# Kernel optimization log

Measured on AMD Instinct MI355X. Metric: run time of the kernel, lower is better.

Reference implementation:

```python
import jax, jax.numpy as jnp
from jax import lax
import numpy as np

B, M = 16384, 200            # flattened batch (B*TT), tokens per observation
NUM_LAYERS, GW, GH = 22, 11, 11
CNN_CH, HIDDEN = 128, 512
ACTION_NVEC = (9, 10)

MAX_VEC = jnp.array([9.0, 1.0, 1.0, 10.0, 3.0, 254.0, 1.0, 1.0, 235.0, 8.0, 9.0,
                     250.0, 29.0, 1.0, 1.0, 8.0, 1.0, 1.0, 6.0, 3.0, 1.0, 2.0],
                    jnp.float32)[None, :, None, None]  # [1,22,1,1]


def setup_inputs() -> dict:
    key = jax.random.key(0)
    ks = jax.random.split(key, 16)
    # compose coords byte so x,y nibbles are valid grid indices (0..10)
    xs = jax.random.randint(ks[0], (B, M), 0, GW)
    ys = jax.random.randint(ks[1], (B, M), 0, GH)
    coords = xs * 16 + ys
    atr = jax.random.randint(ks[2], (B, M), 0, NUM_LAYERS)
    val = jax.random.randint(ks[3], (B, M), 0, 11)
    observations = jnp.stack([coords, atr, val], axis=-1).astype(jnp.int32)  # [B,M,3]

    def nrm(k, shape, std=0.02):
        return (jax.random.normal(k, shape, jnp.float32) * std)

    return {
        "observations": observations,
        "conv1_w": nrm(ks[4], (CNN_CH, NUM_LAYERS, 5, 5)),
        "conv1_b": jnp.zeros((CNN_CH,), jnp.float32),
        "conv2_w": nrm(ks[5], (CNN_CH, CNN_CH, 3, 3)),
        "conv2_b": jnp.zeros((CNN_CH,), jnp.float32),
        "fc_w": nrm(ks[6], (HIDDEN // 2, CNN_CH)),
        "fc_b": jnp.zeros((HIDDEN // 2,), jnp.float32),
        "self_w": nrm(ks[7], (HIDDEN // 2, NUM_LAYERS)),
        "self_b": jnp.zeros((HIDDEN // 2,), jnp.float32),
        "actor0_w": nrm(ks[8], (ACTION_NVEC[0], HIDDEN), std=0.01),
        "actor0_b": jnp.zeros((ACTION_NVEC[0],), jnp.float32),
        "actor1_w": nrm(ks[9], (ACTION_NVEC[1], HIDDEN), std=0.01),
        "actor1_b": jnp.zeros((ACTION_NVEC[1],), jnp.float32),
        "value_w": nrm(ks[10], (1, HIDDEN)),
        "value_b": jnp.zeros((1,), jnp.float32),
    }


def reference(observations, conv1_w, conv1_b, conv2_w, conv2_b, fc_w, fc_b,
              self_w, self_b, actor0_w, actor0_b, actor1_w, actor1_b,
              value_w, value_b):
    obs = jnp.where(observations == 255, 0, observations)
    coords = obs[..., 0]
    xs = (coords >> 4) & 15
    ys = coords & 15
    atr = obs[..., 1]
    vals = obs[..., 2].astype(jnp.float32)           # [B,M]
    Bt = obs.shape[0]
    b_idx = jnp.broadcast_to(jnp.arange(Bt)[:, None], vals.shape)
    # masked scatter into dense grid (all tokens valid after 255->0 clamp)
    box = jnp.zeros((Bt, NUM_LAYERS, GW, GH), jnp.float32)
    box = box.at[b_idx, atr, xs, ys].set(vals, mode="drop")
    feats = box / MAX_VEC                            # [B,22,11,11]

    self_f = jax.nn.relu(feats[:, :, 5, 5] @ self_w.T + self_b)  # [B,256]

    dn = ("NCHW", "OIHW", "NCHW")
    h = lax.conv_general_dilated(feats, conv1_w, (3, 3), "VALID", dimension_numbers=dn)
    h = jax.nn.relu(h + conv1_b[None, :, None, None])            # [B,128,3,3]
    h = lax.conv_general_dilated(h, conv2_w, (1, 1), "VALID", dimension_numbers=dn)
    h = jax.nn.relu(h + conv2_b[None, :, None, None])            # [B,128,1,1]
    h = h.reshape(Bt, -1)
    cnn_f = jax.nn.relu(h @ fc_w.T + fc_b)                       # [B,256]

    hidden = jnp.concatenate([self_f, cnn_f], axis=1)            # [B,512]
    logits0 = hidden @ actor0_w.T + actor0_b
    logits1 = hidden @ actor1_w.T + actor1_b
    value = hidden @ value_w.T + value_b
    return (logits0, logits1, value)
```

## Files before the change

### kernel.cpp

```cpp
#include <hip/hip_runtime.h>

typedef unsigned short u16;
typedef __attribute__((ext_vector_type(8))) short short8;
typedef __attribute__((ext_vector_type(4))) float f32x4;

#define MFMA16(a, b, c) __builtin_amdgcn_mfma_f32_16x16x32_bf16((a), (b), (c), 0, 0, 0)

__device__ __forceinline__ u16 f2bf(float f) {
    unsigned u = __float_as_uint(f);
    unsigned r = (u + 0x7FFFu + ((u >> 16) & 1u)) >> 16;
    return (u16)r;
}

__device__ const float MAXV[22] = {9.f, 1.f, 1.f, 10.f, 3.f, 254.f, 1.f, 1.f, 235.f, 8.f, 9.f,
                                   250.f, 29.f, 1.f, 1.f, 8.f, 1.f, 1.f, 6.f, 3.f, 1.f, 2.f};

__global__ void prep_kernel(
    const float* c1w, const float* c1b, const float* c2w, const float* c2b,
    const float* fcw, const float* fcb, const float* sfw, const float* sfb,
    const float* a0w, const float* a0b, const float* a1w, const float* a1b,
    const float* vw, const float* vb,
    u16* W1F, u16* W2F, u16* FCF, u16* SELFF, u16* HEADF, float* BIAS)
{
    int idx = blockIdx.x * 256 + threadIdx.x;
    if (idx < 73728) {
        int grp = idx >> 9, off = idx & 511;
        int g = grp / 18, ks = grp - g * 18;
        int l = off >> 3, e = off & 7;
        int n = g * 16 + (l & 15);
        int k = ks * 32 + ((l >> 4) << 3) + e;
        float v = 0.f;
        if (k < 550) { int c = k / 25; v = c1w[n * 550 + k] * (1.0f / MAXV[c]); }
        W1F[idx] = f2bf(v);
    } else if (idx < 221184) {
        int j = idx - 73728;
        int grp = j >> 9, off = j & 511;
        int g = grp / 36, ks = grp - g * 36;
        int l = off >> 3, e = off & 7;
        int oc = g * 16 + (l & 15);
        int k = ks * 32 + ((l >> 4) << 3) + e;
        W2F[j] = f2bf(c2w[oc * 1152 + (k & 127) * 9 + (k >> 7)]);
    } else if (idx < 253952) {
        int j = idx - 221184;
        int grp = j >> 9, off = j & 511;
        int g = grp >> 2, kc = grp & 3;
        int l = off >> 3, e = off & 7;
        int n = g * 16 + (l & 15);
        int k = kc * 32 + ((l >> 4) << 3) + e;
        FCF[j] = f2bf(fcw[n * 128 + k]);
    } else if (idx < 262144) {
        int j = idx - 253952;
        int g = j >> 9, off = j & 511;
        int l = off >> 3, e = off & 7;
        int n = g * 16 + (l & 15);
        int k = ((l >> 4) << 3) + e;
        float v = (k < 22) ? sfw[n * 22 + k] * (1.0f / MAXV[k]) : 0.f;
        SELFF[j] = f2bf(v);
    } else if (idx < 278528) {
        int j = idx - 262144;
        int grp = j >> 9, off = j & 511;
        int g = grp >> 4, ks = grp & 15;
        int l = off >> 3, e = off & 7;
        int n = g * 16 + (l & 15);
        int k = ks * 32 + ((l >> 4) << 3) + e;
        float v = 0.f;
        if (n < 9) v = a0w[n * 512 + k];
        else if (n < 19) v = a1w[(n - 9) * 512 + k];
        else if (n == 19) v = vw[k];
        HEADF[j] = f2bf(v);
    } else if (idx < 279328) {
        int j = idx - 278528;
        float v = 0.f;
        if (j < 128) v = c1b[j];
        else if (j < 256) v = c2b[j - 128];
        else if (j < 512) v = fcb[j - 256];
        else if (j < 768) v = sfb[j - 512];
        else {
            int j2 = j - 768;
            if (j2 < 9) v = a0b[j2]; else if (j2 < 19) v = a1b[j2 - 9]; else if (j2 == 19) v = vb[0];
        }
        BIAS[j] = v;
    }
}

__global__ __launch_bounds__(256, 3) void k12_kernel(
    const int* __restrict__ obs, const u16* __restrict__ W1F,
    const float* __restrict__ BIAS, u16* __restrict__ h1F, u16* __restrict__ s22g)
{
    __shared__ __align__(16) u16 A[36 * 576];
    __shared__ __align__(16) int box[2664];
    __shared__ u16 s22[128];
    const int tid = threadIdx.x, w = tid >> 6, l = tid & 63;
    const int s0 = blockIdx.x * 4;

    int tok[4][3];
    if (tid < 200) {
        #pragma unroll
        for (int p = 0; p < 4; ++p) {
            const int* tp = obs + (long)(s0 + p) * 600 + tid * 3;
            tok[p][0] = tp[0]; tok[p][1] = tp[1]; tok[p][2] = tp[2];
        }
    }

    {
        short8 z = {0, 0, 0, 0, 0, 0, 0, 0};
        for (int i = tid; i < 2592; i += 256) *(short8*)(A + i * 8) = z;
        int4 zz = {0, 0, 0, 0};
        for (int i = tid; i < 666; i += 256) ((int4*)box)[i] = zz;
        if (tid < 128) s22[tid] = 0;
    }
    __syncthreads();

    #pragma unroll
    for (int p = 0; p < 4; ++p) {
        int ce = 0, en = 0, va = 0, xa = 0, ya = 0, aa = 0, ok = 0;
        if (tid < 200) {
            int c = tok[p][0], a = tok[p][1], v = tok[p][2];
            c = (c == 255) ? 0 : c; a = (a == 255) ? 0 : a; v = (v == 255) ? 0 : v;
            int xs = (c >> 4) & 15, ys = c & 15;
            ok = ((unsigned)a < 22u) & (xs < 11) & (ys < 11);
            ce = a * 121 + xs * 11 + ys;
            en = ((p + 1) << 16) | (tid << 8) | (v & 255);
            va = v; xa = xs; ya = ys; aa = a;
            if (ok) atomicMax(&box[ce], en);
        }
        __syncthreads();
        if (ok && box[ce] == en) {
            u16 bv = f2bf((float)va);
            if (xa == 5 && ya == 5) s22[p * 32 + aa] = bv;
            int bcol = aa * 25;
            #pragma unroll
            for (int ox = 0; ox < 3; ++ox) {
                int kx = xa - 3 * ox;
                if ((unsigned)kx > 4u) continue;
                #pragma unroll
                for (int oy = 0; oy < 3; ++oy) {
                    int ky = ya - 3 * oy;
                    if ((unsigned)ky > 4u) continue;
                    int row = p * 9 + ox * 3 + oy;
                    int byte = ((row * 576 + bcol + kx * 5 + ky) << 1) ^ ((row & 7) << 4);
                    *(u16*)((char*)A + byte) = bv;
                }
            }
        }
        __syncthreads();
    }
    if (tid < 128) s22g[s0 * 32 + tid] = s22[tid];

    int Aoff[3][2];
    #pragma unroll
    for (int mt = 0; mt < 3; ++mt) {
        int row = mt * 16 + (l & 15);
        row = row < 36 ? row : 35;
        int koff = (l >> 4) << 3;
        Aoff[mt][0] = ((row * 576 + koff) << 1) ^ ((row & 7) << 4);
        Aoff[mt][1] = ((row * 576 + 32 + koff) << 1) ^ ((row & 7) << 4);
    }
    const u16* Wp0 = W1F + ((w * 2 + 0) * 18 << 9) + l * 8;
    const u16* Wp1 = W1F + ((w * 2 + 1) * 18 << 9) + l * 8;

    f32x4 acc[3][2];
    const f32x4 fz = {0.f, 0.f, 0.f, 0.f};
    #pragma unroll
    for (int i = 0; i < 3; ++i) { acc[i][0] = fz; acc[i][1] = fz; }

    short8 cb0 = *(const short8*)(Wp0);
    short8 cb1 = *(const short8*)(Wp1);
    short8 nb0 = *(const short8*)(Wp0 + 512);
    short8 nb1 = *(const short8*)(Wp1 + 512);
    __builtin_amdgcn_s_setprio(1);
    #pragma unroll
    for (int ks = 0; ks < 18; ++ks) {
        short8 t0 = cb0, t1 = cb1;
        if (ks < 16) {
            t0 = *(const short8*)(Wp0 + (ks + 2) * 512);
            t1 = *(const short8*)(Wp1 + (ks + 2) * 512);
        }
        short8 a0 = *(const short8*)((const char*)A + Aoff[0][ks & 1] + (ks >> 1) * 128);
        short8 a1 = *(const short8*)((const char*)A + Aoff[1][ks & 1] + (ks >> 1) * 128);
        short8 a2 = *(const short8*)((const char*)A + Aoff[2][ks & 1] + (ks >> 1) * 128);
        acc[0][0] = MFMA16(a0, cb0, acc[0][0]);
        acc[0][1] = MFMA16(a0, cb1, acc[0][1]);
        acc[1][0] = MFMA16(a1, cb0, acc[1][0]);
        acc[1][1] = MFMA16(a1, cb1, acc[1][1]);
        acc[2][0] = MFMA16(a2, cb0, acc[2][0]);
        acc[2][1] = MFMA16(a2, cb1, acc[2][1]);
        cb0 = nb0; cb1 = nb1; nb0 = t0; nb1 = t1;
    }
    __builtin_amdgcn_s_setprio(0);

    u16* R = (u16*)box;
    #pragma unroll
    for (int mt = 0; mt < 3; ++mt) {
        #pragma unroll
        for (int nt = 0; nt < 2; ++nt) {
            int col = w * 32 + nt * 16 + (l & 15);
            float bias = BIAS[col];
            int hif = nt * 2 + ((l & 15) >> 3);
            int ef = l & 7;
            #pragma unroll
            for (int r = 0; r < 4; ++r) {
                int row = mt * 16 + ((l >> 4) << 2) + r;
                if (row < 36) {
                    int ds = row / 9;
                    int pos = row - ds * 9;
                    int ks = pos * 4 + w;
                    float v = acc[mt][nt][r] + bias;
                    v = v > 0.f ? v : 0.f;
                    R[(ks * 16 + hif * 4 + ds) * 8 + ef] = f2bf(v);
                }
            }
        }
    }
    __syncthreads();
    {
        const long Cbase = (long)(s0 >> 4) * 18432 + (s0 & 15) * 8;
        #pragma unroll
        for (int q = 0; q < 3; ++q) {
            int slot = tid + q * 256;
            if (slot < 576) {
                int ks = slot >> 4, lf = slot & 15;
                *(short8*)(h1F + Cbase + ks * 512 + (lf >> 2) * 128 + (lf & 3) * 8) =
                    *(const short8*)(R + slot * 8);
            }
        }
    }
}

__global__ __launch_bounds__(256, 2) void k3_kernel(
    const u16* __restrict__ h1F, const u16* __restrict__ s22g,
    const u16* __restrict__ W2F, const u16* __restrict__ FCF,
    const u16* __restrict__ SELFF, const u16* __restrict__ HEADF,
    const float* __restrict__ BIAS, float* __restrict__ out, int B)
{
    __shared__ __align__(16) u16 A3[32 * 136];
    __shared__ __align__(16) u16 HID[32 * 520];
    const int tid = threadIdx.x, w = tid >> 6, l = tid & 63;
    const int s0 = blockIdx.x * 32;
    const int sb = blockIdx.x * 2;
    const float* c2b = BIAS + 128;
    const float* fcb = BIAS + 256;
    const float* sfb = BIAS + 512;
    const float* hdb = BIAS + 768;
    const f32x4 fz = {0.f, 0.f, 0.f, 0.f};

    f32x4 acc[2][2];
    acc[0][0] = fz; acc[0][1] = fz; acc[1][0] = fz; acc[1][1] = fz;
    const u16* A0p = h1F + (long)(sb + 0) * 18432 + l * 8;
    const u16* A1p = h1F + (long)(sb + 1) * 18432 + l * 8;
    const u16* B0p = W2F + ((w * 2 + 0) * 36 << 9) + l * 8;
    const u16* B1p = W2F + ((w * 2 + 1) * 36 << 9) + l * 8;

    short8 ca0 = *(const short8*)(A0p), ca1 = *(const short8*)(A1p);
    short8 cb0 = *(const short8*)(B0p), cb1 = *(const short8*)(B1p);
    short8 na0 = *(const short8*)(A0p + 512), na1 = *(const short8*)(A1p + 512);
    short8 nb0 = *(const short8*)(B0p + 512), nb1 = *(const short8*)(B1p + 512);
    __builtin_amdgcn_s_setprio(1);
    #pragma unroll
    for (int ks = 0; ks < 36; ++ks) {
        short8 t0 = ca0, t1 = ca1, t2 = cb0, t3 = cb1;
        if (ks < 34) {
            t0 = *(const short8*)(A0p + (ks + 2) * 512);
            t1 = *(const short8*)(A1p + (ks + 2) * 512);
            t2 = *(const short8*)(B0p + (ks + 2) * 512);
            t3 = *(const short8*)(B1p + (ks + 2) * 512);
        }
        acc[0][0] = MFMA16(ca0, cb0, acc[0][0]);
        acc[0][1] = MFMA16(ca0, cb1, acc[0][1]);
        acc[1][0] = MFMA16(ca1, cb0, acc[1][0]);
        acc[1][1] = MFMA16(ca1, cb1, acc[1][1]);
        ca0 = na0; ca1 = na1; cb0 = nb0; cb1 = nb1;
        na0 = t0; na1 = t1; nb0 = t2; nb1 = t3;
    }
    __builtin_amdgcn_s_setprio(0);
    {
        #pragma unroll
        for (int mt = 0; mt < 2; ++mt)
            #pragma unroll
            for (int nt = 0; nt < 2; ++nt) {
                int col = w * 32 + nt * 16 + (l & 15);
                float bias = c2b[col];
                #pragma unroll
                for (int r = 0; r < 4; ++r) {
                    int row = mt * 16 + ((l >> 4) << 2) + r;
                    float v = acc[mt][nt][r] + bias; v = v > 0.f ? v : 0.f;
                    A3[row * 136 + col] = f2bf(v);
                }
            }
    }
    __syncthreads();

    f32x4 acc8[2][4];
    #pragma unroll
    for (int i = 0; i < 2; ++i)
        #pragma unroll
        for (int j = 0; j < 4; ++j) acc8[i][j] = fz;
    #pragma unroll
    for (int kc = 0; kc < 4; ++kc) {
        short8 bf[4];
        #pragma unroll
        for (int nt = 0; nt < 4; ++nt)
            bf[nt] = *(const short8*)(FCF + (((w * 4 + nt) * 4 + kc) << 9) + l * 8);
        #pragma unroll
        for (int mt = 0; mt < 2; ++mt) {
            short8 a = *(const short8*)(A3 + (mt * 16 + (l & 15)) * 136 + kc * 32 + ((l >> 4) << 3));
            #pragma unroll
            for (int nt = 0; nt < 4; ++nt) acc8[mt][nt] = MFMA16(a, bf[nt], acc8[mt][nt]);
        }
    }
    {
        #pragma unroll
        for (int mt = 0; mt < 2; ++mt)
            #pragma unroll
            for (int nt = 0; nt < 4; ++nt) {
                int col = w * 64 + nt * 16 + (l & 15);
                float bias = fcb[col];
                #pragma unroll
                for (int r = 0; r < 4; ++r) {
                    int row = mt * 16 + ((l >> 4) << 2) + r;
                    float v = acc8[mt][nt][r] + bias; v = v > 0.f ? v : 0.f;
                    HID[row * 520 + 256 + col] = f2bf(v);
                }
            }
    }

    {
        f32x4 acc9[2][4];
        #pragma unroll
        for (int i = 0; i < 2; ++i)
            #pragma unroll
            for (int j = 0; j < 4; ++j) acc9[i][j] = fz;
        short8 bs[4];
        #pragma unroll
        for (int nt = 0; nt < 4; ++nt)
            bs[nt] = *(const short8*)(SELFF + ((w * 4 + nt) << 9) + l * 8);
        #pragma unroll
        for (int mt = 0; mt < 2; ++mt) {
            short8 a = *(const short8*)(s22g + (s0 + mt * 16 + (l & 15)) * 32 + ((l >> 4) << 3));
            #pragma unroll
            for (int nt = 0; nt < 4; ++nt) acc9[mt][nt] = MFMA16(a, bs[nt], acc9[mt][nt]);
        }
        #pragma unroll
        for (int mt = 0; mt < 2; ++mt)
            #pragma unroll
            for (int nt = 0; nt < 4; ++nt) {
                int col = w * 64 + nt * 16 + (l & 15);
                float bias = sfb[col];
                #pragma unroll
                for (int r = 0; r < 4; ++r) {
                    int row = mt * 16 + ((l >> 4) << 2) + r;
                    float v = acc9[mt][nt][r] + bias; v = v > 0.f ? v : 0.f;
                    HID[row * 520 + col] = f2bf(v);
                }
            }
    }
    __syncthreads();

    f32x4 hacc = fz;
    const int rt = w & 1, ct = w >> 1;
    #pragma unroll
    for (int ks = 0; ks < 16; ++ks) {
        short8 a = *(const short8*)(HID + (rt * 16 + (l & 15)) * 520 + ks * 32 + ((l >> 4) << 3));
        short8 b = *(const short8*)(HEADF + ((ct * 16 + ks) << 9) + l * 8);
        hacc = MFMA16(a, b, hacc);
    }
    #pragma unroll
    for (int r = 0; r < 4; ++r) {
        int srow = s0 + rt * 16 + ((l >> 4) << 2) + r;
        int col = ct * 16 + (l & 15);
        float v = hacc[r] + hdb[col];
        if (col < 9) out[(long)srow * 9 + col] = v;
        else if (col < 19) out[(long)B * 9 + (long)srow * 10 + (col - 9)] = v;
        else if (col == 19) out[(long)B * 19 + srow] = v;
    }
}

extern "C" void kernel_launch(void* const* d_in, const int* in_sizes, int n_in,
                              void* d_out, int out_size, void* d_ws, size_t ws_size,
                              hipStream_t stream)
{
    const int*   obs = (const int*)d_in[0];
    const float* c1w = (const float*)d_in[1];
    const float* c1b = (const float*)d_in[2];
    const float* c2w = (const float*)d_in[3];
    const float* c2b = (const float*)d_in[4];
    const float* fcw = (const float*)d_in[5];
    const float* fcb = (const float*)d_in[6];
    const float* sfw = (const float*)d_in[7];
    const float* sfb = (const float*)d_in[8];
    const float* a0w = (const float*)d_in[9];
    const float* a0b = (const float*)d_in[10];
    const float* a1w = (const float*)d_in[11];
    const float* a1b = (const float*)d_in[12];
    const float* vw  = (const float*)d_in[13];
    const float* vb  = (const float*)d_in[14];
    const int B = in_sizes[0] / 600;

    char* ws = (char*)d_ws;
    u16*   W1F   = (u16*)(ws + 0);
    u16*   W2F   = (u16*)(ws + 147456);
    u16*   FCF   = (u16*)(ws + 442368);
    u16*   SELFF = (u16*)(ws + 507904);
    u16*   HEADF = (u16*)(ws + 524288);
    float* BIAS  = (float*)(ws + 557056);
    u16*   s22g  = (u16*)(ws + 560256);
    u16*   h1F   = (u16*)(ws + 560256 + (size_t)B * 64);

    prep_kernel<<<1092, 256, 0, stream>>>(c1w, c1b, c2w, c2b, fcw, fcb, sfw, sfb,
                                          a0w, a0b, a1w, a1b, vw, vb,
                                          W1F, W2F, FCF, SELFF, HEADF, BIAS);
    k12_kernel<<<B / 4, 256, 0, stream>>>(obs, W1F, BIAS, h1F, s22g);
    k3_kernel<<<B / 32, 256, 0, stream>>>(h1F, s22g, W2F, FCF, SELFF, HEADF, BIAS,
                                          (float*)d_out, B);
}
```

Before: 75.94 us.

## Give each wave its own scatter sample and halve k3 tile to 16 rows

In k12, each wave now owns one sample: it scatters its tokens into a per-wave scratch region that serves first as the dedup box and then as the im2col tile. This replaces the four block-wide barrier rounds with wave-local work and shrinks shared memory. In k3, each block processes 16 samples instead of 32, uses a 3-deep prefetch pipeline, and raises the occupancy target to 4 blocks; only two waves run the head GEMM. The trade-off is less weight reuse per block in k3 and reliance on wave-internal ordering of LDS atomics without a barrier.

```diff
diff --git a/kernel.cpp b/kernel.cpp
--- a/kernel.cpp
+++ b/kernel.cpp
@@ -87,74 +87,78 @@
     const int* __restrict__ obs, const u16* __restrict__ W1F,
     const float* __restrict__ BIAS, u16* __restrict__ h1F, u16* __restrict__ s22g)
 {
-    __shared__ __align__(16) u16 A[36 * 576];
-    __shared__ __align__(16) int box[2664];
+    __shared__ __align__(16) u16 Ablk[4 * 5328];
     __shared__ u16 s22[128];
     const int tid = threadIdx.x, w = tid >> 6, l = tid & 63;
     const int s0 = blockIdx.x * 4;
-
-    int tok[4][3];
-    if (tid < 200) {
-        #pragma unroll
-        for (int p = 0; p < 4; ++p) {
-            const int* tp = obs + (long)(s0 + p) * 600 + tid * 3;
-            tok[p][0] = tp[0]; tok[p][1] = tp[1]; tok[p][2] = tp[2];
-        }
-    }
-
-    {
-        short8 z = {0, 0, 0, 0, 0, 0, 0, 0};
-        for (int i = tid; i < 2592; i += 256) *(short8*)(A + i * 8) = z;
-        int4 zz = {0, 0, 0, 0};
-        for (int i = tid; i < 666; i += 256) ((int4*)box)[i] = zz;
-        if (tid < 128) s22[tid] = 0;
-    }
-    __syncthreads();
-
-    #pragma unroll
-    for (int p = 0; p < 4; ++p) {
-        int ce = 0, en = 0, va = 0, xa = 0, ya = 0, aa = 0, ok = 0;
-        if (tid < 200) {
-            int c = tok[p][0], a = tok[p][1], v = tok[p][2];
-            c = (c == 255) ? 0 : c; a = (a == 255) ? 0 : a; v = (v == 255) ? 0 : v;
-            int xs = (c >> 4) & 15, ys = c & 15;
-            ok = ((unsigned)a < 22u) & (xs < 11) & (ys < 11);
-            ce = a * 121 + xs * 11 + ys;
-            en = ((p + 1) << 16) | (tid << 8) | (v & 255);
-            va = v; xa = xs; ya = ys; aa = a;
-            if (ok) atomicMax(&box[ce], en);
-        }
-        __syncthreads();
-        if (ok && box[ce] == en) {
-            u16 bv = f2bf((float)va);
-            if (xa == 5 && ya == 5) s22[p * 32 + aa] = bv;
-            int bcol = aa * 25;
+    const short8 z8 = {0, 0, 0, 0, 0, 0, 0, 0};
+
+    const int* myobs = obs + (long)(s0 + w) * 600;
+    int tk[4][3];
+    #pragma unroll
+    for (int r = 0; r < 4; ++r) {
+        int m = r * 64 + l; m = m < 200 ? m : 0;
+        tk[r][0] = myobs[m * 3]; tk[r][1] = myobs[m * 3 + 1]; tk[r][2] = myobs[m * 3 + 2];
+    }
+    if (l < 32) s22[w * 32 + l] = 0;
+
+    u16* blk = Ablk + w * 5328;
+    for (int i = l; i < 666; i += 64) *(short8*)(blk + i * 8) = z8;
+
+    int* boxW = (int*)blk;
+    int ce[4], en[4], ok[4], va[4], xa[4], ya[4], aa[4], win[4];
+    #pragma unroll
+    for (int r = 0; r < 4; ++r) {
+        int m = r * 64 + l;
+        int c = tk[r][0], a = tk[r][1], v = tk[r][2];
+        c = (c == 255) ? 0 : c; a = (a == 255) ? 0 : a; v = (v == 255) ? 0 : v;
+        int xs = (c >> 4) & 15, ys = c & 15;
+        ok[r] = (m < 200) & ((unsigned)a < 22u) & (xs < 11) & (ys < 11);
+        ce[r] = ok[r] ? (a * 121 + xs * 11 + ys) : 0;
+        en[r] = ((m + 1) << 8) | (v & 255);
+        va[r] = v; xa[r] = xs; ya[r] = ys; aa[r] = a;
+        if (ok[r]) atomicMax(&boxW[ce[r]], en[r]);
+    }
+    __builtin_amdgcn_sched_barrier(0);
+    #pragma unroll
+    for (int r = 0; r < 4; ++r) win[r] = ok[r] & (boxW[ce[r]] == en[r]);
+    __builtin_amdgcn_sched_barrier(0);
+    for (int i = l; i < 666; i += 64) *(short8*)(blk + i * 8) = z8;
+    __builtin_amdgcn_sched_barrier(0);
+    #pragma unroll
+    for (int r = 0; r < 4; ++r) {
+        if (win[r]) {
+            u16 bv = f2bf((float)va[r]);
+            if (xa[r] == 5 && ya[r] == 5) s22[w * 32 + aa[r]] = bv;
+            int bcol = aa[r] * 25;
             #pragma unroll
             for (int ox = 0; ox < 3; ++ox) {
-                int kx = xa - 3 * ox;
+                int kx = xa[r] - 3 * ox;
                 if ((unsigned)kx > 4u) continue;
                 #pragma unroll
                 for (int oy = 0; oy < 3; ++oy) {
-                    int ky = ya - 3 * oy;
+                    int ky = ya[r] - 3 * oy;
                     if ((unsigned)ky > 4u) continue;
-                    int row = p * 9 + ox * 3 + oy;
-                    int byte = ((row * 576 + bcol + kx * 5 + ky) << 1) ^ ((row & 7) << 4);
-                    *(u16*)((char*)A + byte) = bv;
+                    int pos = ox * 3 + oy;
+                    int row = w * 9 + pos;
+                    int off = (((pos * 576 + bcol + kx * 5 + ky)) << 1) ^ ((row & 7) << 4);
+                    *(u16*)((char*)blk + off) = bv;
                 }
             }
         }
-        __syncthreads();
-    }
-    if (tid < 128) s22g[s0 * 32 + tid] = s22[tid];
-
-    int Aoff[3][2];
+    }
+    if (l < 32) s22g[(s0 + w) * 32 + l] = s22[w * 32 + l];
+    __syncthreads();
+
+    int addr[3][2];
     #pragma unroll
     for (int mt = 0; mt < 3; ++mt) {
         int row = mt * 16 + (l & 15);
         row = row < 36 ? row : 35;
+        int ls = row / 9, pos = row - ls * 9;
         int koff = (l >> 4) << 3;
-        Aoff[mt][0] = ((row * 576 + koff) << 1) ^ ((row & 7) << 4);
-        Aoff[mt][1] = ((row * 576 + 32 + koff) << 1) ^ ((row & 7) << 4);
+        addr[mt][0] = ls * 10656 + (((pos * 576 + koff) << 1) ^ ((row & 7) << 4));
+        addr[mt][1] = ls * 10656 + (((pos * 576 + 32 + koff) << 1) ^ ((row & 7) << 4));
     }
     const u16* Wp0 = W1F + ((w * 2 + 0) * 18 << 9) + l * 8;
     const u16* Wp1 = W1F + ((w * 2 + 1) * 18 << 9) + l * 8;
@@ -176,9 +180,9 @@
             t0 = *(const short8*)(Wp0 + (ks + 2) * 512);
             t1 = *(const short8*)(Wp1 + (ks + 2) * 512);
         }
-        short8 a0 = *(const short8*)((const char*)A + Aoff[0][ks & 1] + (ks >> 1) * 128);
-        short8 a1 = *(const short8*)((const char*)A + Aoff[1][ks & 1] + (ks >> 1) * 128);
-        short8 a2 = *(const short8*)((const char*)A + Aoff[2][ks & 1] + (ks >> 1) * 128);
+        short8 a0 = *(const short8*)((const char*)Ablk + addr[0][ks & 1] + (ks >> 1) * 128);
+        short8 a1 = *(const short8*)((const char*)Ablk + addr[1][ks & 1] + (ks >> 1) * 128);
+        short8 a2 = *(const short8*)((const char*)Ablk + addr[2][ks & 1] + (ks >> 1) * 128);
         acc[0][0] = MFMA16(a0, cb0, acc[0][0]);
         acc[0][1] = MFMA16(a0, cb1, acc[0][1]);
         acc[1][0] = MFMA16(a1, cb0, acc[1][0]);
@@ -188,8 +192,9 @@
         cb0 = nb0; cb1 = nb1; nb0 = t0; nb1 = t1;
     }
     __builtin_amdgcn_s_setprio(0);
-
-    u16* R = (u16*)box;
+    __syncthreads();
+
+    u16* R = Ablk;
     #pragma unroll
     for (int mt = 0; mt < 3; ++mt) {
         #pragma unroll
@@ -227,151 +232,133 @@
     }
 }
 
-__global__ __launch_bounds__(256, 2) void k3_kernel(
+__global__ __launch_bounds__(256, 4) void k3_kernel(
     const u16* __restrict__ h1F, const u16* __restrict__ s22g,
     const u16* __restrict__ W2F, const u16* __restrict__ FCF,
     const u16* __restrict__ SELFF, const u16* __restrict__ HEADF,
     const float* __restrict__ BIAS, float* __restrict__ out, int B)
 {
-    __shared__ __align__(16) u16 A3[32 * 136];
-    __shared__ __align__(16) u16 HID[32 * 520];
+    __shared__ __align__(16) u16 A3[16 * 136];
+    __shared__ __align__(16) u16 HID[16 * 520];
     const int tid = threadIdx.x, w = tid >> 6, l = tid & 63;
-    const int s0 = blockIdx.x * 32;
-    const int sb = blockIdx.x * 2;
+    const int s0 = blockIdx.x * 16;
     const float* c2b = BIAS + 128;
     const float* fcb = BIAS + 256;
     const float* sfb = BIAS + 512;
     const float* hdb = BIAS + 768;
     const f32x4 fz = {0.f, 0.f, 0.f, 0.f};
 
-    f32x4 acc[2][2];
-    acc[0][0] = fz; acc[0][1] = fz; acc[1][0] = fz; acc[1][1] = fz;
-    const u16* A0p = h1F + (long)(sb + 0) * 18432 + l * 8;
-    const u16* A1p = h1F + (long)(sb + 1) * 18432 + l * 8;
+    const u16* Ap  = h1F + (long)blockIdx.x * 18432 + l * 8;
     const u16* B0p = W2F + ((w * 2 + 0) * 36 << 9) + l * 8;
     const u16* B1p = W2F + ((w * 2 + 1) * 36 << 9) + l * 8;
-
-    short8 ca0 = *(const short8*)(A0p), ca1 = *(const short8*)(A1p);
-    short8 cb0 = *(const short8*)(B0p), cb1 = *(const short8*)(B1p);
-    short8 na0 = *(const short8*)(A0p + 512), na1 = *(const short8*)(A1p + 512);
-    short8 nb0 = *(const short8*)(B0p + 512), nb1 = *(const short8*)(B1p + 512);
+    f32x4 acc0 = fz, acc1 = fz;
+    short8 pa[3], pb0[3], pb1[3];
+    #pragma unroll
+    for (int d = 0; d < 3; ++d) {
+        pa[d]  = *(const short8*)(Ap + d * 512);
+        pb0[d] = *(const short8*)(B0p + d * 512);
+        pb1[d] = *(const short8*)(B1p + d * 512);
+    }
     __builtin_amdgcn_s_setprio(1);
     #pragma unroll
-    for (int ks = 0; ks < 36; ++ks) {
-        short8 t0 = ca0, t1 = ca1, t2 = cb0, t3 = cb1;
-        if (ks < 34) {
-            t0 = *(const short8*)(A0p + (ks + 2) * 512);
-            t1 = *(const short8*)(A1p + (ks + 2) * 512);
-            t2 = *(const short8*)(B0p + (ks + 2) * 512);
-            t3 = *(const short8*)(B1p + (ks + 2) * 512);
-        }
-        acc[0][0] = MFMA16(ca0, cb0, acc[0][0]);
-        acc[0][1] = MFMA16(ca0, cb1, acc[0][1]);
-        acc[1][0] = MFMA16(ca1, cb0, acc[1][0]);
-        acc[1][1] = MFMA16(ca1, cb1, acc[1][1]);
-        ca0 = na0; ca1 = na1; cb0 = nb0; cb1 = nb1;
-        na0 = t0; na1 = t1; nb0 = t2; nb1 = t3;
+    for (int g = 0; g < 12; ++g) {
+        #pragma unroll
+        for (int d = 0; d < 3; ++d) {
+            int ks = g * 3 + d;
+            short8 a = pa[d], b0 = pb0[d], b1 = pb1[d];
+            if (ks < 33) {
+                pa[d]  = *(const short8*)(Ap + (ks + 3) * 512);
+                pb0[d] = *(const short8*)(B0p + (ks + 3) * 512);
+                pb1[d] = *(const short8*)(B1p + (ks + 3) * 512);
+            }
+            acc0 = MFMA16(a, b0, acc0);
+            acc1 = MFMA16(a, b1, acc1);
+        }
     }
     __builtin_amdgcn_s_setprio(0);
     {
         #pragma unroll
-        for (int mt = 0; mt < 2; ++mt)
+        for (int nt = 0; nt < 2; ++nt) {
+            int col = w * 32 + nt * 16 + (l & 15);
+            float bias = c2b[col];
+            const f32x4& a4 = nt ? acc1 : acc0;
             #pragma unroll
-            for (int nt = 0; nt < 2; ++nt) {
-                int col = w * 32 + nt * 16 + (l & 15);
-                float bias = c2b[col];
-                #pragma unroll
-                for (int r = 0; r < 4; ++r) {
-                    int row = mt * 16 + ((l >> 4) << 2) + r;
-                    float v = acc[mt][nt][r] + bias; v = v > 0.f ? v : 0.f;
-                    A3[row * 136 + col] = f2bf(v);
-                }
-            }
+            for (int r = 0; r < 4; ++r) {
+                int row = ((l >> 4) << 2) + r;
+                float v = a4[r] + bias; v = v > 0.f ? v : 0.f;
+                A3[row * 136 + col] = f2bf(v);
+            }
+        }
     }
     __syncthreads();
 
-    f32x4 acc8[2][4];
-    #pragma unroll
-    for (int i = 0; i < 2; ++i)
-        #pragma unroll
-        for (int j = 0; j < 4; ++j) acc8[i][j] = fz;
+    f32x4 acc8[4];
+    #pragma unroll
+    for (int j = 0; j < 4; ++j) acc8[j] = fz;
     #pragma unroll
     for (int kc = 0; kc < 4; ++kc) {
         short8 bf[4];
         #pragma unroll
         for (int nt = 0; nt < 4; ++nt)
             bf[nt] = *(const short8*)(FCF + (((w * 4 + nt) * 4 + kc) << 9) + l * 8);
-        #pragma unroll
-        for (int mt = 0; mt < 2; ++mt) {
-            short8 a = *(const short8*)(A3 + (mt * 16 + (l & 15)) * 136 + kc * 32 + ((l >> 4) << 3));
-            #pragma unroll
-            for (int nt = 0; nt < 4; ++nt) acc8[mt][nt] = MFMA16(a, bf[nt], acc8[mt][nt]);
-        }
-    }
+        short8 a = *(const short8*)(A3 + (l & 15) * 136 + kc * 32 + ((l >> 4) << 3));
+        #pragma unroll
+        for (int nt = 0; nt < 4; ++nt) acc8[nt] = MFMA16(a, bf[nt], acc8[nt]);
+    }
+    #pragma unroll
+    for (int nt = 0; nt < 4; ++nt) {
+        int col = w * 64 + nt * 16 + (l & 15);
+        float bias = fcb[col];
+        #pragma unroll
+        for (int r = 0; r < 4; ++r) {
+            int row = ((l >> 4) << 2) + r;
+            float v = acc8[nt][r] + bias; v = v > 0.f ? v : 0.f;
+            HID[row * 520 + 256 + col] = f2bf(v);
+        }
+    }
+
     {
-        #pragma unroll
-        for (int mt = 0; mt < 2; ++mt)
-            #pragma unroll
-            for (int nt = 0; nt < 4; ++nt) {
-                int col = w * 64 + nt * 16 + (l & 15);
-                float bias = fcb[col];
-                #pragma unroll
-                for (int r = 0; r < 4; ++r) {
-                    int row = mt * 16 + ((l >> 4) << 2) + r;
-                    float v = acc8[mt][nt][r] + bias; v = v > 0.f ? v : 0.f;
-                    HID[row * 520 + 256 + col] = f2bf(v);
-                }
-            }
-    }
-
-    {
-        f32x4 acc9[2][4];
-        #pragma unroll
-        for (int i = 0; i < 2; ++i)
-            #pragma unroll
-            for (int j = 0; j < 4; ++j) acc9[i][j] = fz;
+        f32x4 acc9[4];
+        #pragma unroll
+        for (int j = 0; j < 4; ++j) acc9[j] = fz;
         short8 bs[4];
         #pragma unroll
         for (int nt = 0; nt < 4; ++nt)
             bs[nt] = *(const short8*)(SELFF + ((w * 4 + nt) << 9) + l * 8);
-        #pragma unroll
-        for (int mt = 0; mt < 2; ++mt) {
-            short8 a = *(const short8*)(s22g + (s0 + mt * 16 + (l & 15)) * 32 + ((l >> 4) << 3));
+        short8 a = *(const short8*)(s22g + (s0 + (l & 15)) * 32 + ((l >> 4) << 3));
+        #pragma unroll
+        for (int nt = 0; nt < 4; ++nt) acc9[nt] = MFMA16(a, bs[nt], acc9[nt]);
+        #pragma unroll
+        for (int nt = 0; nt < 4; ++nt) {
+            int col = w * 64 + nt * 16 + (l & 15);
+            float bias = sfb[col];
             #pragma unroll
-            for (int nt = 0; nt < 4; ++nt) acc9[mt][nt] = MFMA16(a, bs[nt], acc9[mt][nt]);
-        }
-        #pragma unroll
-        for (int mt = 0; mt < 2; ++mt)
-            #pragma unroll
-            for (int nt = 0; nt < 4; ++nt) {
-                int col = w * 64 + nt * 16 + (l & 15);
-                float bias = sfb[col];
-                #pragma unroll
-                for (int r = 0; r < 4; ++r) {
-                    int row = mt * 16 + ((l >> 4) << 2) + r;
-                    float v = acc9[mt][nt][r] + bias; v = v > 0.f ? v : 0.f;
-                    HID[row * 520 + col] = f2bf(v);
-                }
-            }
+            for (int r = 0; r < 4; ++r) {
+                int row = ((l >> 4) << 2) + r;
+                float v = acc9[nt][r] + bias; v = v > 0.f ? v : 0.f;
+                HID[row * 520 + col] = f2bf(v);
+            }
+        }
     }
     __syncthreads();
 
-    f32x4 hacc = fz;
-    const int rt = w & 1, ct = w >> 1;
-    #pragma unroll
-    for (int ks = 0; ks < 16; ++ks) {
-        short8 a = *(const short8*)(HID + (rt * 16 + (l & 15)) * 520 + ks * 32 + ((l >> 4) << 3));
-        short8 b = *(const short8*)(HEADF + ((ct * 16 + ks) << 9) + l * 8);
-        hacc = MFMA16(a, b, hacc);
-    }
-    #pragma unroll
-    for (int r = 0; r < 4; ++r) {
-        int srow = s0 + rt * 16 + ((l >> 4) << 2) + r;
-        int col = ct * 16 + (l & 15);
-        float v = hacc[r] + hdb[col];
-        if (col < 9) out[(long)srow * 9 + col] = v;
-        else if (col < 19) out[(long)B * 9 + (long)srow * 10 + (col - 9)] = v;
-        else if (col == 19) out[(long)B * 19 + srow] = v;
+    if (w < 2) {
+        f32x4 hacc = fz;
+        #pragma unroll
+        for (int ks = 0; ks < 16; ++ks) {
+            short8 a = *(const short8*)(HID + (l & 15) * 520 + ks * 32 + ((l >> 4) << 3));
+            short8 b = *(const short8*)(HEADF + ((w * 16 + ks) << 9) + l * 8);
+            hacc = MFMA16(a, b, hacc);
+        }
+        #pragma unroll
+        for (int r = 0; r < 4; ++r) {
+            int srow = s0 + ((l >> 4) << 2) + r;
+            int col = w * 16 + (l & 15);
+            float v = hacc[r] + hdb[col];
+            if (col < 9) out[(long)srow * 9 + col] = v;
+            else if (col < 19) out[(long)B * 9 + (long)srow * 10 + (col - 9)] = v;
+            else if (col == 19) out[(long)B * 19 + srow] = v;
+        }
     }
 }
 
@@ -410,6 +397,6 @@
                                           a0w, a0b, a1w, a1b, vw, vb,
                                           W1F, W2F, FCF, SELFF, HEADF, BIAS);
     k12_kernel<<<B / 4, 256, 0, stream>>>(obs, W1F, BIAS, h1F, s22g);
-    k3_kernel<<<B / 32, 256, 0, stream>>>(h1F, s22g, W2F, FCF, SELFF, HEADF, BIAS,
+    k3_kernel<<<B / 16, 256, 0, stream>>>(h1F, s22g, W2F, FCF, SELFF, HEADF, BIAS,
                                           (float*)d_out, B);
 }
```

Result: slower. 79.31 us (+4.4%).

## Split conv2 and FC/head stages into separate kernels via global MFMA-layout buffer

Applied to the files above, without the earlier changes.

Splits the fused conv2+FC+self+head kernel into two kernels. The first does the conv2 GEMM and writes the ReLU'd bf16 activations to a global buffer in MFMA fragment layout. The second processes 16 samples per block with higher occupancy for the FC, self and head GEMMs. The aim is more parallelism and occupancy in the tail stages, at the cost of an extra launch and a global round trip of the intermediate activations.

```diff
diff --git a/kernel.cpp b/kernel.cpp
--- a/kernel.cpp
+++ b/kernel.cpp
@@ -227,25 +227,17 @@
     }
 }
 
-__global__ __launch_bounds__(256, 2) void k3_kernel(
-    const u16* __restrict__ h1F, const u16* __restrict__ s22g,
-    const u16* __restrict__ W2F, const u16* __restrict__ FCF,
-    const u16* __restrict__ SELFF, const u16* __restrict__ HEADF,
-    const float* __restrict__ BIAS, float* __restrict__ out, int B)
+__global__ __launch_bounds__(256, 2) void k3a_kernel(
+    const u16* __restrict__ h1F, const u16* __restrict__ W2F,
+    const float* __restrict__ BIAS, u16* __restrict__ a3F)
 {
-    __shared__ __align__(16) u16 A3[32 * 136];
-    __shared__ __align__(16) u16 HID[32 * 520];
     const int tid = threadIdx.x, w = tid >> 6, l = tid & 63;
-    const int s0 = blockIdx.x * 32;
-    const int sb = blockIdx.x * 2;
+    const int sb = blockIdx.x * 2, s0 = blockIdx.x * 32;
     const float* c2b = BIAS + 128;
-    const float* fcb = BIAS + 256;
-    const float* sfb = BIAS + 512;
-    const float* hdb = BIAS + 768;
     const f32x4 fz = {0.f, 0.f, 0.f, 0.f};
-
     f32x4 acc[2][2];
     acc[0][0] = fz; acc[0][1] = fz; acc[1][0] = fz; acc[1][1] = fz;
+
     const u16* A0p = h1F + (long)(sb + 0) * 18432 + l * 8;
     const u16* A1p = h1F + (long)(sb + 1) * 18432 + l * 8;
     const u16* B0p = W2F + ((w * 2 + 0) * 36 << 9) + l * 8;
@@ -273,105 +265,105 @@
         na0 = t0; na1 = t1; nb0 = t2; nb1 = t3;
     }
     __builtin_amdgcn_s_setprio(0);
+
+    #pragma unroll
+    for (int mt = 0; mt < 2; ++mt) {
+        #pragma unroll
+        for (int nt = 0; nt < 2; ++nt) {
+            int col = w * 32 + nt * 16 + (l & 15);
+            float bias = c2b[col];
+            #pragma unroll
+            for (int r = 0; r < 4; ++r) {
+                int row = mt * 16 + ((l >> 4) << 2) + r;
+                int s = s0 + row;
+                float v = acc[mt][nt][r] + bias; v = v > 0.f ? v : 0.f;
+                long ad = (long)(s >> 4) * 2048 + (col >> 5) * 512 +
+                          (s & 15) * 8 + (((col >> 3) & 3) << 7) + (col & 7);
+                a3F[ad] = f2bf(v);
+            }
+        }
+    }
+}
+
+__global__ __launch_bounds__(256, 4) void k3b_kernel(
+    const u16* __restrict__ a3F, const u16* __restrict__ s22g,
+    const u16* __restrict__ FCF, const u16* __restrict__ SELFF,
+    const u16* __restrict__ HEADF, const float* __restrict__ BIAS,
+    float* __restrict__ out, int B)
+{
+    __shared__ __align__(16) u16 HID[16 * 520];
+    const int tid = threadIdx.x, w = tid >> 6, l = tid & 63;
+    const int s0 = blockIdx.x * 16;
+    const float* fcb = BIAS + 256;
+    const float* sfb = BIAS + 512;
+    const float* hdb = BIAS + 768;
+    const f32x4 fz = {0.f, 0.f, 0.f, 0.f};
+
+    f32x4 acc8[4];
+    #pragma unroll
+    for (int j = 0; j < 4; ++j) acc8[j] = fz;
+    #pragma unroll
+    for (int kc = 0; kc < 4; ++kc) {
+        short8 a = *(const short8*)(a3F + (long)blockIdx.x * 2048 + kc * 512 + l * 8);
+        #pragma unroll
+        for (int nt = 0; nt < 4; ++nt) {
+            short8 bf = *(const short8*)(FCF + (((w * 4 + nt) * 4 + kc) << 9) + l * 8);
+            acc8[nt] = MFMA16(a, bf, acc8[nt]);
+        }
+    }
+    #pragma unroll
+    for (int nt = 0; nt < 4; ++nt) {
+        int col = w * 64 + nt * 16 + (l & 15);
+        float bias = fcb[col];
+        #pragma unroll
+        for (int r = 0; r < 4; ++r) {
+            int row = ((l >> 4) << 2) + r;
+            float v = acc8[nt][r] + bias; v = v > 0.f ? v : 0.f;
+            HID[row * 520 + 256 + col] = f2bf(v);
+        }
+    }
+
     {
-        #pragma unroll
-        for (int mt = 0; mt < 2; ++mt)
+        f32x4 acc9[4];
+        #pragma unroll
+        for (int j = 0; j < 4; ++j) acc9[j] = fz;
+        short8 a = *(const short8*)(s22g + (s0 + (l & 15)) * 32 + ((l >> 4) << 3));
+        #pragma unroll
+        for (int nt = 0; nt < 4; ++nt) {
+            short8 bs = *(const short8*)(SELFF + ((w * 4 + nt) << 9) + l * 8);
+            acc9[nt] = MFMA16(a, bs, acc9[nt]);
+        }
+        #pragma unroll
+        for (int nt = 0; nt < 4; ++nt) {
+            int col = w * 64 + nt * 16 + (l & 15);
+            float bias = sfb[col];
             #pragma unroll
-            for (int nt = 0; nt < 2; ++nt) {
-                int col = w * 32 + nt * 16 + (l & 15);
-                float bias = c2b[col];
-                #pragma unroll
-                for (int r = 0; r < 4; ++r) {
-                    int row = mt * 16 + ((l >> 4) << 2) + r;
-                    float v = acc[mt][nt][r] + bias; v = v > 0.f ? v : 0.f;
-                    A3[row * 136 + col] = f2bf(v);
-                }
+            for (int r = 0; r < 4; ++r) {
+                int row = ((l >> 4) << 2) + r;
+                float v = acc9[nt][r] + bias; v = v > 0.f ? v : 0.f;
+                HID[row * 520 + col] = f2bf(v);
             }
+        }
     }
     __syncthreads();
 
-    f32x4 acc8[2][4];
-    #pragma unroll
-    for (int i = 0; i < 2; ++i)
-        #pragma unroll
-        for (int j = 0; j < 4; ++j) acc8[i][j] = fz;
-    #pragma unroll
-    for (int kc = 0; kc < 4; ++kc) {
-        short8 bf[4];
-        #pragma unroll
-        for (int nt = 0; nt < 4; ++nt)
-            bf[nt] = *(const short8*)(FCF + (((w * 4 + nt) * 4 + kc) << 9) + l * 8);
-        #pragma unroll
-        for (int mt = 0; mt < 2; ++mt) {
-            short8 a = *(const short8*)(A3 + (mt * 16 + (l & 15)) * 136 + kc * 32 + ((l >> 4) << 3));
-            #pragma unroll
-            for (int nt = 0; nt < 4; ++nt) acc8[mt][nt] = MFMA16(a, bf[nt], acc8[mt][nt]);
-        }
-    }
-    {
-        #pragma unroll
-        for (int mt = 0; mt < 2; ++mt)
-            #pragma unroll
-            for (int nt = 0; nt < 4; ++nt) {
-                int col = w * 64 + nt * 16 + (l & 15);
-                float bias = fcb[col];
-                #pragma unroll
-                for (int r = 0; r < 4; ++r) {
-                    int row = mt * 16 + ((l >> 4) << 2) + r;
-                    float v = acc8[mt][nt][r] + bias; v = v > 0.f ? v : 0.f;
-                    HID[row * 520 + 256 + col] = f2bf(v);
-                }
-            }
-    }
-
-    {
-        f32x4 acc9[2][4];
-        #pragma unroll
-        for (int i = 0; i < 2; ++i)
-            #pragma unroll
-            for (int j = 0; j < 4; ++j) acc9[i][j] = fz;
-        short8 bs[4];
-        #pragma unroll
-        for (int nt = 0; nt < 4; ++nt)
-            bs[nt] = *(const short8*)(SELFF + ((w * 4 + nt) << 9) + l * 8);
-        #pragma unroll
-        for (int mt = 0; mt < 2; ++mt) {
-            short8 a = *(const short8*)(s22g + (s0 + mt * 16 + (l & 15)) * 32 + ((l >> 4) << 3));
-            #pragma unroll
-            for (int nt = 0; nt < 4; ++nt) acc9[mt][nt] = MFMA16(a, bs[nt], acc9[mt][nt]);
-        }
-        #pragma unroll
-        for (int mt = 0; mt < 2; ++mt)
-            #pragma unroll
-            for (int nt = 0; nt < 4; ++nt) {
-                int col = w * 64 + nt * 16 + (l & 15);
-                float bias = sfb[col];
-                #pragma unroll
-                for (int r = 0; r < 4; ++r) {
-                    int row = mt * 16 + ((l >> 4) << 2) + r;
-                    float v = acc9[mt][nt][r] + bias; v = v > 0.f ? v : 0.f;
-                    HID[row * 520 + col] = f2bf(v);
-                }
-            }
-    }
-    __syncthreads();
-
-    f32x4 hacc = fz;
-    const int rt = w & 1, ct = w >> 1;
-    #pragma unroll
-    for (int ks = 0; ks < 16; ++ks) {
-        short8 a = *(const short8*)(HID + (rt * 16 + (l & 15)) * 520 + ks * 32 + ((l >> 4) << 3));
-        short8 b = *(const short8*)(HEADF + ((ct * 16 + ks) << 9) + l * 8);
-        hacc = MFMA16(a, b, hacc);
-    }
-    #pragma unroll
-    for (int r = 0; r < 4; ++r) {
-        int srow = s0 + rt * 16 + ((l >> 4) << 2) + r;
-        int col = ct * 16 + (l & 15);
-        float v = hacc[r] + hdb[col];
-        if (col < 9) out[(long)srow * 9 + col] = v;
-        else if (col < 19) out[(long)B * 9 + (long)srow * 10 + (col - 9)] = v;
-        else if (col == 19) out[(long)B * 19 + srow] = v;
+    if (w < 2) {
+        f32x4 hacc = fz;
+        #pragma unroll
+        for (int ks = 0; ks < 16; ++ks) {
+            short8 a = *(const short8*)(HID + (l & 15) * 520 + ks * 32 + ((l >> 4) << 3));
+            short8 b = *(const short8*)(HEADF + ((w * 16 + ks) << 9) + l * 8);
+            hacc = MFMA16(a, b, hacc);
+        }
+        #pragma unroll
+        for (int r = 0; r < 4; ++r) {
+            int srow = s0 + ((l >> 4) << 2) + r;
+            int col = w * 16 + (l & 15);
+            float v = hacc[r] + hdb[col];
+            if (col < 9) out[(long)srow * 9 + col] = v;
+            else if (col < 19) out[(long)B * 9 + (long)srow * 10 + (col - 9)] = v;
+            else if (col == 19) out[(long)B * 19 + srow] = v;
+        }
     }
 }
 
@@ -405,11 +397,13 @@
     float* BIAS  = (float*)(ws + 557056);
     u16*   s22g  = (u16*)(ws + 560256);
     u16*   h1F   = (u16*)(ws + 560256 + (size_t)B * 64);
+    u16*   a3F   = (u16*)(ws + 560256 + (size_t)B * 64 + (size_t)B * 2304);
 
     prep_kernel<<<1092, 256, 0, stream>>>(c1w, c1b, c2w, c2b, fcw, fcb, sfw, sfb,
                                           a0w, a0b, a1w, a1b, vw, vb,
                                           W1F, W2F, FCF, SELFF, HEADF, BIAS);
     k12_kernel<<<B / 4, 256, 0, stream>>>(obs, W1F, BIAS, h1F, s22g);
-    k3_kernel<<<B / 32, 256, 0, stream>>>(h1F, s22g, W2F, FCF, SELFF, HEADF, BIAS,
-                                          (float*)d_out, B);
-}
+    k3a_kernel<<<B / 32, 256, 0, stream>>>(h1F, W2F, BIAS, a3F);
+    k3b_kernel<<<B / 16, 256, 0, stream>>>(a3F, s22g, FCF, SELFF, HEADF, BIAS,
+                                           (float*)d_out, B);
+}
```

After: 79.22 us. 4.3% more time.
